# Kernel tuning notes

Measured on AMD Instinct MI355X. Metric: run time of the kernel, lower is better.

## Reference

```python
import jax, jax.numpy as jnp
import numpy as np

BLOCK = 128          # block_size in the source
FP8_MAX = 448.0      # max representable magnitude of float8_e4m3fn


def _quant_weight(w):
    """Pre-quantize a [N, K] float weight into fp8 values + per 128x128 block scales."""
    N, K = w.shape
    wb = w.reshape(N // BLOCK, BLOCK, K // BLOCK, BLOCK)
    w_scale = jnp.max(jnp.abs(wb), axis=(1, 3)) / FP8_MAX           # [Nb, Kb]
    s = jnp.where(w_scale == 0, 1.0, w_scale)
    wq = (wb / s[:, None, :, None]).astype(jnp.float8_e4m3fn).astype(jnp.float32)
    return wq.reshape(N, K), w_scale


def setup_inputs() -> dict:
    key = jax.random.key(0)
    kx, kw = jax.random.split(key)
    M, K, N = 16384, 2048, 2048
    x = jax.random.normal(kx, (M, K), dtype=jnp.float32)
    w = jax.random.normal(kw, (N, K), dtype=jnp.float32) * 0.02
    w_fp8, w_scale = _quant_weight(w)
    return {"x": x, "w_fp8": w_fp8, "w_scale": w_scale}


def reference(x, w_fp8, w_scale):
    """fp8 block-quantized linear: act_quant(x) then dequantized GEMM.

    x:       [M, K] float32 activations
    w_fp8:   [N, K] fp8-valued weight (stored as float32, exactly e4m3 representable)
    w_scale: [N/128, K/128] per-block weight scales
    """
    M, K = x.shape
    N = w_fp8.shape[0]
    # --- act_quant: per 128-element block along K, scale = amax / 448 ---
    xb = x.reshape(M, K // BLOCK, BLOCK)
    x_scale = jnp.max(jnp.abs(xb), axis=-1) / FP8_MAX               # [M, Kb]
    sx = jnp.where(x_scale == 0, 1.0, x_scale)
    xq = (xb / sx[..., None]).astype(jnp.float8_e4m3fn).astype(jnp.float32)
    # --- fp8_gemm with inline dequant: scales factor out per (m-block, n-block, k-block)
    # sum_kb sx[m,kb]*sw[nb,kb]*(xq . wq) == (xq*sx) @ (wq*sw)^T exactly ---
    x_deq = (xq * sx[..., None]).reshape(M, K)
    w_deq = (w_fp8.reshape(N // BLOCK, BLOCK, K // BLOCK, BLOCK)
             * w_scale[:, None, :, None]).reshape(N, K)
    return x_deq @ w_deq.T                                          # [M, N]
```

## Files before the change

### kernel.cpp

```cpp
#include <hip/hip_runtime.h>

#define M_DIM 16384
#define N_DIM 2048
#define K_DIM 2048
#define KB    (K_DIM / 128)

#define BM 256
#define BN 256
#define BK 64
#define NT (K_DIM / BK)

#define XGRID (M_DIM * K_DIM / 2048)
#define WGRID (N_DIM * K_DIM / 2048)

typedef __bf16 bf16x8 __attribute__((ext_vector_type(8)));
typedef float  f32x4  __attribute__((ext_vector_type(4)));

__device__ __forceinline__ unsigned short f32_to_bf16_rne(float f) {
    unsigned int u = __float_as_uint(f);
    u += 0x7FFFu + ((u >> 16) & 1u);
    return (unsigned short)(u >> 16);
}

__global__ __launch_bounds__(256) void quant_all_kernel(const float* __restrict__ x,
                                                        unsigned short* __restrict__ xdq,
                                                        const float* __restrict__ w,
                                                        const float* __restrict__ wscale,
                                                        unsigned short* __restrict__ wdq) {
    const int tid = threadIdx.x;
    if (blockIdx.x < XGRID) {
        const size_t base = ((size_t)blockIdx.x * 256 + tid) * 8;
        const float4 va = *(const float4*)(x + base);
        const float4 vb = *(const float4*)(x + base + 4);
        float amax = fmaxf(
            fmaxf(fmaxf(fabsf(va.x), fabsf(va.y)), fmaxf(fabsf(va.z), fabsf(va.w))),
            fmaxf(fmaxf(fabsf(vb.x), fabsf(vb.y)), fmaxf(fabsf(vb.z), fabsf(vb.w))));
#pragma unroll
        for (int m = 8; m >= 1; m >>= 1)
            amax = fmaxf(amax, __shfl_xor(amax, m, 64));
        float s = amax / 448.0f;
        if (s == 0.0f) s = 1.0f;
        const int p01 = __builtin_amdgcn_cvt_pk_fp8_f32(va.x / s, va.y / s, 0, false);
        const int p23 = __builtin_amdgcn_cvt_pk_fp8_f32(va.z / s, va.w / s, 0, false);
        const int p45 = __builtin_amdgcn_cvt_pk_fp8_f32(vb.x / s, vb.y / s, 0, false);
        const int p67 = __builtin_amdgcn_cvt_pk_fp8_f32(vb.z / s, vb.w / s, 0, false);
        uint4 out;
        out.x = (unsigned int)f32_to_bf16_rne(__builtin_amdgcn_cvt_f32_fp8(p01, 0) * s)
              | ((unsigned int)f32_to_bf16_rne(__builtin_amdgcn_cvt_f32_fp8(p01, 1) * s) << 16);
        out.y = (unsigned int)f32_to_bf16_rne(__builtin_amdgcn_cvt_f32_fp8(p23, 0) * s)
              | ((unsigned int)f32_to_bf16_rne(__builtin_amdgcn_cvt_f32_fp8(p23, 1) * s) << 16);
        out.z = (unsigned int)f32_to_bf16_rne(__builtin_amdgcn_cvt_f32_fp8(p45, 0) * s)
              | ((unsigned int)f32_to_bf16_rne(__builtin_amdgcn_cvt_f32_fp8(p45, 1) * s) << 16);
        out.w = (unsigned int)f32_to_bf16_rne(__builtin_amdgcn_cvt_f32_fp8(p67, 0) * s)
              | ((unsigned int)f32_to_bf16_rne(__builtin_amdgcn_cvt_f32_fp8(p67, 1) * s) << 16);
        *(uint4*)(xdq + base) = out;
    } else {
        const size_t e = ((size_t)(blockIdx.x - XGRID) * 256 + tid) * 8;
        const float4 va = *(const float4*)(w + e);
        const float4 vb = *(const float4*)(w + e + 4);
        const int n = (int)(e >> 11);
        const int k = (int)(e & 2047);
        const float s = wscale[(n >> 7) * KB + (k >> 7)];
        uint4 out;
        out.x = (unsigned int)f32_to_bf16_rne(va.x * s) | ((unsigned int)f32_to_bf16_rne(va.y * s) << 16);
        out.y = (unsigned int)f32_to_bf16_rne(va.z * s) | ((unsigned int)f32_to_bf16_rne(va.w * s) << 16);
        out.z = (unsigned int)f32_to_bf16_rne(vb.x * s) | ((unsigned int)f32_to_bf16_rne(vb.y * s) << 16);
        out.w = (unsigned int)f32_to_bf16_rne(vb.z * s) | ((unsigned int)f32_to_bf16_rne(vb.w * s) << 16);
        *(uint4*)(wdq + e) = out;
    }
}

__global__ __launch_bounds__(512, 2) void gemm_bt_kernel(const unsigned short* __restrict__ A,
                                                         const unsigned short* __restrict__ B,
                                                         float* __restrict__ C) {
    __shared__ __align__(16) unsigned short As[2][2][256][32];
    __shared__ __align__(16) unsigned short Bs[2][2][256][32];

    const int tid  = threadIdx.x;
    const int lane = tid & 63;
    const int wave = tid >> 6;
    const int wm   = (wave >> 2) * 128;
    const int wn   = (wave & 3) * 64;
    const int quad = lane >> 4;
    const int l16  = lane & 15;
    const int pc   = quad ^ ((l16 >> 1) & 3);

    const int m0 = blockIdx.x * BM;
    const int n0 = blockIdx.y * BN;

    f32x4 acc[8][4] = {};

    const int srow = tid >> 2;
    const int sc   = (tid & 3) ^ ((tid >> 3) & 3);
    const unsigned short* gA = A + (size_t)(m0 + srow) * K_DIM + sc * 8;
    const unsigned short* gB = B + (size_t)(n0 + srow) * K_DIM + sc * 8;

#define GLD(SRC, DST) __builtin_amdgcn_global_load_lds( \
    (__attribute__((address_space(1))) void*)(SRC), \
    (__attribute__((address_space(3))) void*)(DST), 16, 0, 0)

#define STG_A(DB, KH, KT) do { \
    GLD(gA + (size_t)(KT) * 64 + (KH) * 32,                       &As[DB][KH][wave * 16][0]); \
    GLD(gA + (size_t)128 * K_DIM + (size_t)(KT) * 64 + (KH) * 32, &As[DB][KH][128 + wave * 16][0]); \
  } while (0)
#define STG_B(DB, KH, KT) do { \
    GLD(gB + (size_t)(KT) * 64 + (KH) * 32,                       &Bs[DB][KH][wave * 16][0]); \
    GLD(gB + (size_t)128 * K_DIM + (size_t)(KT) * 64 + (KH) * 32, &Bs[DB][KH][128 + wave * 16][0]); \
  } while (0)

#define VMCNT(n) asm volatile("s_waitcnt vmcnt(" #n ")" ::: "memory")
#define BAR() __builtin_amdgcn_s_barrier()
#define LGKM0() do { \
    asm volatile("s_waitcnt lgkmcnt(0)" ::: "memory"); \
    __builtin_amdgcn_sched_barrier(0); \
  } while (0)

#define LDA(BUF, KH, i) (*(const bf16x8*)(&As[BUF][KH][wm + (i) * 16 + l16][pc * 8]))
#define LDB(BUF, KH, j) (*(const bf16x8*)(&Bs[BUF][KH][wn + (j) * 16 + l16][pc * 8]))

#define MM16(I0) do { \
    __builtin_amdgcn_s_setprio(1); \
    _Pragma("unroll") \
    for (int i = 0; i < 4; ++i) { \
      _Pragma("unroll") \
      for (int j = 0; j < 4; ++j) \
        acc[(I0) + i][j] = __builtin_amdgcn_mfma_f32_16x16x32_bf16(af[i], bf[j], acc[(I0) + i][j], 0, 0, 0); \
    } \
    __builtin_amdgcn_s_setprio(0); \
  } while (0)

#define TILE(BUF, S0, S1, S2, S3, W1, W3) do { \
    bf16x8 af[4], bf[4]; \
    af[0] = LDA(BUF, 0, 0); af[1] = LDA(BUF, 0, 1); af[2] = LDA(BUF, 0, 2); af[3] = LDA(BUF, 0, 3); \
    bf[0] = LDB(BUF, 0, 0); bf[1] = LDB(BUF, 0, 1); bf[2] = LDB(BUF, 0, 2); bf[3] = LDB(BUF, 0, 3); \
    S0; BAR(); LGKM0(); MM16(0); BAR(); \
    af[0] = LDA(BUF, 0, 4); af[1] = LDA(BUF, 0, 5); af[2] = LDA(BUF, 0, 6); af[3] = LDA(BUF, 0, 7); \
    S1; BAR(); LGKM0(); MM16(4); W1; BAR(); \
    af[0] = LDA(BUF, 1, 0); af[1] = LDA(BUF, 1, 1); af[2] = LDA(BUF, 1, 2); af[3] = LDA(BUF, 1, 3); \
    bf[0] = LDB(BUF, 1, 0); bf[1] = LDB(BUF, 1, 1); bf[2] = LDB(BUF, 1, 2); bf[3] = LDB(BUF, 1, 3); \
    S2; BAR(); LGKM0(); MM16(0); BAR(); \
    af[0] = LDA(BUF, 1, 4); af[1] = LDA(BUF, 1, 5); af[2] = LDA(BUF, 1, 6); af[3] = LDA(BUF, 1, 7); \
    S3; BAR(); LGKM0(); MM16(4); W3; BAR(); \
  } while (0)

    STG_A(0, 0, 0); STG_B(0, 0, 0);
    STG_A(0, 1, 0); STG_B(0, 1, 0);
    STG_A(1, 0, 1); STG_B(1, 0, 1);
    VMCNT(8);
    BAR();

#pragma unroll 1
    for (int t = 0; t < NT - 2; t += 2) {
        TILE(0, STG_A(1, 1, t + 1), STG_B(1, 1, t + 1),
                STG_A(0, 0, t + 2), STG_B(0, 0, t + 2), VMCNT(8), VMCNT(8));
        TILE(1, STG_A(0, 1, t + 2), STG_B(0, 1, t + 2),
                STG_A(1, 0, t + 3), STG_B(1, 0, t + 3), VMCNT(8), VMCNT(8));
    }
    TILE(0, STG_A(1, 1, NT - 1), STG_B(1, 1, NT - 1), (void)0, (void)0, VMCNT(8), VMCNT(4));
    TILE(1, (void)0, (void)0, (void)0, (void)0, VMCNT(0), (void)0);

#pragma unroll
    for (int i = 0; i < 8; ++i) {
        const int row = m0 + wm + i * 16 + quad * 4;
#pragma unroll
        for (int j = 0; j < 4; ++j) {
            const int col = n0 + wn + j * 16 + l16;
            float* cp = C + (size_t)row * N_DIM + col;
#pragma unroll
            for (int r = 0; r < 4; ++r)
                cp[(size_t)r * N_DIM] = acc[i][j][r];
        }
    }
}

extern "C" void kernel_launch(void* const* d_in, const int* in_sizes, int n_in,
                              void* d_out, int out_size, void* d_ws, size_t ws_size,
                              hipStream_t stream) {
    const float* x      = (const float*)d_in[0];
    const float* wfp8   = (const float*)d_in[1];
    const float* wscale = (const float*)d_in[2];
    float* out = (float*)d_out;

    unsigned short* xdq = (unsigned short*)d_ws;
    unsigned short* wdq = xdq + (size_t)M_DIM * K_DIM;

    quant_all_kernel<<<XGRID + WGRID, 256, 0, stream>>>(x, xdq, wfp8, wscale, wdq);
    gemm_bt_kernel<<<dim3(M_DIM / BM, N_DIM / BN), 512, 0, stream>>>(xdq, wdq, out);
}
```

Before: 358.4 us.

## Software-pipeline LDS fragment reads with inline-asm ds_read and partial lgkmcnt waits

```diff
diff --git a/kernel.cpp b/kernel.cpp
--- a/kernel.cpp
+++ b/kernel.cpp
@@ -15,6 +15,7 @@
 
 typedef __bf16 bf16x8 __attribute__((ext_vector_type(8)));
 typedef float  f32x4  __attribute__((ext_vector_type(4)));
+typedef int    i32x4  __attribute__((ext_vector_type(4)));
 
 __device__ __forceinline__ unsigned short f32_to_bf16_rne(float f) {
     unsigned int u = __float_as_uint(f);
@@ -110,37 +111,71 @@
 
 #define VMCNT(n) asm volatile("s_waitcnt vmcnt(" #n ")" ::: "memory")
 #define BAR() __builtin_amdgcn_s_barrier()
-#define LGKM0() do { \
-    asm volatile("s_waitcnt lgkmcnt(0)" ::: "memory"); \
+#define LGKM(n) do { \
+    asm volatile("s_waitcnt lgkmcnt(" #n ")" ::: "memory"); \
     __builtin_amdgcn_sched_barrier(0); \
   } while (0)
 
-#define LDA(BUF, KH, i) (*(const bf16x8*)(&As[BUF][KH][wm + (i) * 16 + l16][pc * 8]))
-#define LDB(BUF, KH, j) (*(const bf16x8*)(&Bs[BUF][KH][wn + (j) * 16 + l16][pc * 8]))
-
-#define MM16(I0) do { \
+    i32x4 ae0, ae1, ae2, ae3, be0, be1, be2, be3;
+    i32x4 ao0, ao1, ao2, ao3, bo0, bo1, bo2, bo3;
+    i32x4 ax0, ax1, ax2, ax3;
+
+    const unsigned aA = (unsigned)(unsigned long long)
+        (__attribute__((address_space(3))) const void*)&As[0][0][wm + l16][pc * 8];
+    const unsigned aB = (unsigned)(unsigned long long)
+        (__attribute__((address_space(3))) const void*)&Bs[0][0][wn + l16][pc * 8];
+
+#define DSR(D, BASE, IMM) \
+    asm volatile("ds_read_b128 %0, %1 offset:%c2" : "=v"(D) : "v"(BASE), "i"(IMM))
+
+#define RD_AX(BUF, KH) do { \
+    DSR(ax0, aA, (BUF) * 32768 + (KH) * 16384 + 4096); \
+    DSR(ax1, aA, (BUF) * 32768 + (KH) * 16384 + 5120); \
+    DSR(ax2, aA, (BUF) * 32768 + (KH) * 16384 + 6144); \
+    DSR(ax3, aA, (BUF) * 32768 + (KH) * 16384 + 7168); \
+  } while (0)
+#define RD_E(BUF, KH) do { \
+    DSR(ae0, aA, (BUF) * 32768 + (KH) * 16384 + 0);    \
+    DSR(ae1, aA, (BUF) * 32768 + (KH) * 16384 + 1024); \
+    DSR(ae2, aA, (BUF) * 32768 + (KH) * 16384 + 2048); \
+    DSR(ae3, aA, (BUF) * 32768 + (KH) * 16384 + 3072); \
+    DSR(be0, aB, (BUF) * 32768 + (KH) * 16384 + 0);    \
+    DSR(be1, aB, (BUF) * 32768 + (KH) * 16384 + 1024); \
+    DSR(be2, aB, (BUF) * 32768 + (KH) * 16384 + 2048); \
+    DSR(be3, aB, (BUF) * 32768 + (KH) * 16384 + 3072); \
+  } while (0)
+#define RD_O(BUF, KH) do { \
+    DSR(ao0, aA, (BUF) * 32768 + (KH) * 16384 + 0);    \
+    DSR(ao1, aA, (BUF) * 32768 + (KH) * 16384 + 1024); \
+    DSR(ao2, aA, (BUF) * 32768 + (KH) * 16384 + 2048); \
+    DSR(ao3, aA, (BUF) * 32768 + (KH) * 16384 + 3072); \
+    DSR(bo0, aB, (BUF) * 32768 + (KH) * 16384 + 0);    \
+    DSR(bo1, aB, (BUF) * 32768 + (KH) * 16384 + 1024); \
+    DSR(bo2, aB, (BUF) * 32768 + (KH) * 16384 + 2048); \
+    DSR(bo3, aB, (BUF) * 32768 + (KH) * 16384 + 3072); \
+  } while (0)
+
+#define BC(X) __builtin_bit_cast(bf16x8, X)
+#define MMROW(I, AF, B0, B1, B2, B3) do { \
+    acc[I][0] = __builtin_amdgcn_mfma_f32_16x16x32_bf16(BC(AF), BC(B0), acc[I][0], 0, 0, 0); \
+    acc[I][1] = __builtin_amdgcn_mfma_f32_16x16x32_bf16(BC(AF), BC(B1), acc[I][1], 0, 0, 0); \
+    acc[I][2] = __builtin_amdgcn_mfma_f32_16x16x32_bf16(BC(AF), BC(B2), acc[I][2], 0, 0, 0); \
+    acc[I][3] = __builtin_amdgcn_mfma_f32_16x16x32_bf16(BC(AF), BC(B3), acc[I][3], 0, 0, 0); \
+  } while (0)
+#define MM16(I0, A0, A1, A2, A3, B0, B1, B2, B3) do { \
     __builtin_amdgcn_s_setprio(1); \
-    _Pragma("unroll") \
-    for (int i = 0; i < 4; ++i) { \
-      _Pragma("unroll") \
-      for (int j = 0; j < 4; ++j) \
-        acc[(I0) + i][j] = __builtin_amdgcn_mfma_f32_16x16x32_bf16(af[i], bf[j], acc[(I0) + i][j], 0, 0, 0); \
-    } \
+    MMROW((I0) + 0, A0, B0, B1, B2, B3); \
+    MMROW((I0) + 1, A1, B0, B1, B2, B3); \
+    MMROW((I0) + 2, A2, B0, B1, B2, B3); \
+    MMROW((I0) + 3, A3, B0, B1, B2, B3); \
     __builtin_amdgcn_s_setprio(0); \
   } while (0)
 
-#define TILE(BUF, S0, S1, S2, S3, W1, W3) do { \
-    bf16x8 af[4], bf[4]; \
-    af[0] = LDA(BUF, 0, 0); af[1] = LDA(BUF, 0, 1); af[2] = LDA(BUF, 0, 2); af[3] = LDA(BUF, 0, 3); \
-    bf[0] = LDB(BUF, 0, 0); bf[1] = LDB(BUF, 0, 1); bf[2] = LDB(BUF, 0, 2); bf[3] = LDB(BUF, 0, 3); \
-    S0; BAR(); LGKM0(); MM16(0); BAR(); \
-    af[0] = LDA(BUF, 0, 4); af[1] = LDA(BUF, 0, 5); af[2] = LDA(BUF, 0, 6); af[3] = LDA(BUF, 0, 7); \
-    S1; BAR(); LGKM0(); MM16(4); W1; BAR(); \
-    af[0] = LDA(BUF, 1, 0); af[1] = LDA(BUF, 1, 1); af[2] = LDA(BUF, 1, 2); af[3] = LDA(BUF, 1, 3); \
-    bf[0] = LDB(BUF, 1, 0); bf[1] = LDB(BUF, 1, 1); bf[2] = LDB(BUF, 1, 2); bf[3] = LDB(BUF, 1, 3); \
-    S2; BAR(); LGKM0(); MM16(0); BAR(); \
-    af[0] = LDA(BUF, 1, 4); af[1] = LDA(BUF, 1, 5); af[2] = LDA(BUF, 1, 6); af[3] = LDA(BUF, 1, 7); \
-    S3; BAR(); LGKM0(); MM16(4); W3; BAR(); \
+#define TILE_STD(B_, KT1, KT2) do { \
+    RD_AX(B_, 0);      STG_A((B_) ^ 1, 1, KT1); LGKM(4); MM16(0, ae0, ae1, ae2, ae3, be0, be1, be2, be3); VMCNT(6); BAR(); \
+    RD_O(B_, 1);       STG_B((B_) ^ 1, 1, KT1); LGKM(8); MM16(4, ax0, ax1, ax2, ax3, be0, be1, be2, be3); BAR(); \
+    RD_AX(B_, 1);      STG_A(B_, 0, KT2);       LGKM(4); MM16(0, ao0, ao1, ao2, ao3, bo0, bo1, bo2, bo3); VMCNT(6); BAR(); \
+    RD_E((B_) ^ 1, 0); STG_B(B_, 0, KT2);       LGKM(8); MM16(4, ax0, ax1, ax2, ax3, bo0, bo1, bo2, bo3); BAR(); \
   } while (0)
 
     STG_A(0, 0, 0); STG_B(0, 0, 0);
@@ -148,16 +183,21 @@
     STG_A(1, 0, 1); STG_B(1, 0, 1);
     VMCNT(8);
     BAR();
+    RD_E(0, 0);
 
 #pragma unroll 1
     for (int t = 0; t < NT - 2; t += 2) {
-        TILE(0, STG_A(1, 1, t + 1), STG_B(1, 1, t + 1),
-                STG_A(0, 0, t + 2), STG_B(0, 0, t + 2), VMCNT(8), VMCNT(8));
-        TILE(1, STG_A(0, 1, t + 2), STG_B(0, 1, t + 2),
-                STG_A(1, 0, t + 3), STG_B(1, 0, t + 3), VMCNT(8), VMCNT(8));
+        TILE_STD(0, t + 1, t + 2);
+        TILE_STD(1, t + 2, t + 3);
     }
-    TILE(0, STG_A(1, 1, NT - 1), STG_B(1, 1, NT - 1), (void)0, (void)0, VMCNT(8), VMCNT(4));
-    TILE(1, (void)0, (void)0, (void)0, (void)0, VMCNT(0), (void)0);
+    RD_AX(0, 0); STG_A(1, 1, NT - 1); LGKM(4); MM16(0, ae0, ae1, ae2, ae3, be0, be1, be2, be3); VMCNT(6); BAR();
+    RD_O(0, 1);  STG_B(1, 1, NT - 1); LGKM(8); MM16(4, ax0, ax1, ax2, ax3, be0, be1, be2, be3); BAR();
+    RD_AX(0, 1);                      LGKM(4); MM16(0, ao0, ao1, ao2, ao3, bo0, bo1, bo2, bo3); VMCNT(4); BAR();
+    RD_E(1, 0);                       LGKM(8); MM16(4, ax0, ax1, ax2, ax3, bo0, bo1, bo2, bo3); BAR();
+    RD_AX(1, 0);                      LGKM(4); MM16(0, ae0, ae1, ae2, ae3, be0, be1, be2, be3); VMCNT(0); BAR();
+    RD_O(1, 1);                       LGKM(8); MM16(4, ax0, ax1, ax2, ax3, be0, be1, be2, be3); BAR();
+    RD_AX(1, 1);                      LGKM(4); MM16(0, ao0, ao1, ao2, ao3, bo0, bo1, bo2, bo3); BAR();
+                                      LGKM(0); MM16(4, ax0, ax1, ax2, ax3, bo0, bo1, bo2, bo3);
 
 #pragma unroll
     for (int i = 0; i < 8; ++i) {
```

Result: faster. 349.9 us (-2.4%).
